# Kernel optimization log

Measured on AMD Instinct MI355X. Metric: run time of the kernel, lower is better.

The kernel has to match this reference:

```python
import jax, jax.numpy as jnp
import numpy as np

D_MODEL = 1024
N_HEADS = 16
HEAD_DIM = D_MODEL // N_HEADS
B, T = 4, 2048


def setup_inputs() -> dict:
    key = jax.random.key(0)
    ks = jax.random.split(key, 5)
    s = D_MODEL ** -0.5
    return {
        "x": jax.random.normal(ks[0], (B, T, D_MODEL), dtype=jnp.float32),
        "Wqkv": jax.random.normal(ks[1], (3 * D_MODEL, D_MODEL), dtype=jnp.float32) * s,
        "bqkv": jax.random.normal(ks[2], (3 * D_MODEL,), dtype=jnp.float32) * 0.01,
        "Wo": jax.random.normal(ks[3], (D_MODEL, D_MODEL), dtype=jnp.float32) * s,
        "bo": jax.random.normal(ks[4], (D_MODEL,), dtype=jnp.float32) * 0.01,
    }


def reference(x, Wqkv, bqkv, Wo, bo):
    b, t, c = x.shape
    h, hd = N_HEADS, HEAD_DIM
    qkv = x @ Wqkv.T + bqkv                      # [B,T,3C]
    # Faithful to source: reshape to [B,T,H,3*hd] THEN chunk -> per-head slices of 3C
    qkv = qkv.reshape(b, t, h, 3 * hd).transpose(0, 2, 1, 3)  # [B,H,T,3hd]
    q, k, v = jnp.split(qkv, 3, axis=-1)          # each [B,H,T,hd]
    scores = jnp.einsum('bhqd,bhkd->bhqk', q, k) * (hd ** -0.5)
    attn = jax.nn.softmax(scores, axis=-1)        # [B,H,T,T]
    out = jnp.einsum('bhqk,bhkd->bhqd', attn, v)  # [B,H,T,hd]
    out = out.transpose(0, 2, 1, 3).reshape(b, t, c)
    return out @ Wo.T + bo
```

## Files before the change

### kernel.cpp

```cpp
#include <hip/hip_runtime.h>
#include <hip/hip_bf16.h>


typedef float f32x4 __attribute__((ext_vector_type(4)));
typedef short s16x8 __attribute__((ext_vector_type(8)));
typedef short s16x4 __attribute__((ext_vector_type(4)));
typedef unsigned int u32x4 __attribute__((ext_vector_type(4)));

#define MFMA(acc, a, b) \
    (acc) = __builtin_amdgcn_mfma_f32_16x16x32_bf16((a), (b), (acc), 0, 0, 0)

__device__ __forceinline__ short f2bb(float f) {
    return (short)__bfloat16_as_ushort(__float2bfloat16(f));
}

__global__ __launch_bounds__(256)
void conv_all(const float* __restrict__ x, const float* __restrict__ Wqkv,
              const float* __restrict__ bqkv, const float* __restrict__ Wo,
              short* __restrict__ xb, short* __restrict__ Wqkvb,
              float* __restrict__ bqkvr, short* __restrict__ Wob)
{
    int blk = blockIdx.x;
    if (blk < 4096) {
        long i = ((long)blk * 256 + threadIdx.x) * 8;
        f32x4 a = *(const f32x4*)(x + i);
        f32x4 b = *(const f32x4*)(x + i + 4);
        s16x8 r;
#pragma unroll
        for (int j = 0; j < 4; j++) { r[j] = f2bb(a[j]); r[4 + j] = f2bb(b[j]); }
        *(s16x8*)(xb + i) = r;
    } else if (blk < 4096 + 3072) {
        int np = blk - 4096;
        int slice = np >> 10, rr = np & 1023;
        int src = (rr >> 6) * 192 + slice * 64 + (rr & 63);
        f32x4 v = *(const f32x4*)(Wqkv + (long)src * 1024 + threadIdx.x * 4);
        s16x4 o;
#pragma unroll
        for (int j = 0; j < 4; j++) o[j] = f2bb(v[j]);
        *(s16x4*)(Wqkvb + (long)np * 1024 + threadIdx.x * 4) = o;
        if (threadIdx.x == 0) bqkvr[np] = bqkv[src];
    } else {
        int n = blk - 4096 - 3072;
        f32x4 v = *(const f32x4*)(Wo + (long)n * 1024 + threadIdx.x * 4);
        s16x4 o;
#pragma unroll
        for (int j = 0; j < 4; j++) o[j] = f2bb(v[j]);
        *(s16x4*)(Wob + (long)n * 1024 + threadIdx.x * 4) = o;
    }
}

__global__ __launch_bounds__(256)
void gemm128(const short* __restrict__ A, const short* __restrict__ W,
             const float* __restrict__ bias,
             short* __restrict__ Cq, short* __restrict__ Ck,
             short* __restrict__ Cv, float* __restrict__ Cf, int proj)
{
    __shared__ short Asw[128 * 64];
    __shared__ short Bsw[128 * 64];
    const int tid = threadIdx.x;
    const int wave = tid >> 6, lane = tid & 63;
    const int quad = lane >> 4, l16 = lane & 15;
    const int m0 = blockIdx.y * 128;
    const int ng = blockIdx.x * 128;
    const int sr = tid >> 3, sc = tid & 7;

    f32x4 acc[4][4] = {};
    s16x8 pav[4], pbv[4];

#pragma unroll
    for (int u = 0; u < 4; u++) {
        int r = u * 32 + sr;
        pav[u] = *(const s16x8*)(A + (long)(m0 + r) * 1024 + sc * 8);
        pbv[u] = *(const s16x8*)(W + (long)(ng + r) * 1024 + sc * 8);
    }

    for (int k0 = 0; k0 < 1024; k0 += 64) {
        __syncthreads();
#pragma unroll
        for (int u = 0; u < 4; u++) {
            int r = u * 32 + sr;
            int slot = sc ^ (r & 7);
            *(s16x8*)&Asw[r * 64 + slot * 8] = pav[u];
            *(s16x8*)&Bsw[r * 64 + slot * 8] = pbv[u];
        }
        __syncthreads();
        if (k0 + 64 < 1024) {
            int kn = k0 + 64;
#pragma unroll
            for (int u = 0; u < 4; u++) {
                int r = u * 32 + sr;
                pav[u] = *(const s16x8*)(A + (long)(m0 + r) * 1024 + kn + sc * 8);
                pbv[u] = *(const s16x8*)(W + (long)(ng + r) * 1024 + kn + sc * 8);
            }
        }

        s16x8 af[2][4], bf[2][4];
#pragma unroll
        for (int ks = 0; ks < 2; ks++)
#pragma unroll
            for (int i = 0; i < 4; i++) {
                int slot = (ks * 4 + quad) ^ (l16 & 7);
                int ra = (wave >> 1) * 64 + i * 16 + l16;
                af[ks][i] = *(const s16x8*)&Asw[ra * 64 + slot * 8];
                int rb = (wave & 1) * 64 + i * 16 + l16;
                bf[ks][i] = *(const s16x8*)&Bsw[rb * 64 + slot * 8];
            }
#pragma unroll
        for (int ks = 0; ks < 2; ks++)
#pragma unroll
            for (int i = 0; i < 4; i++)
#pragma unroll
                for (int j = 0; j < 4; j++)
                    MFMA(acc[i][j], af[ks][i], bf[ks][j]);
    }

    const int slice = ng >> 10;
    const float scale = (!proj && slice == 0) ? 0.125f : 1.0f;
    short* Cb = (slice == 0) ? Cq : (slice == 1) ? Ck : Cv;
    const int nl = ng & 1023;
#pragma unroll
    for (int i = 0; i < 4; i++)
#pragma unroll
        for (int r = 0; r < 4; r++) {
            long m = m0 + (wave >> 1) * 64 + i * 16 + quad * 4 + r;
#pragma unroll
            for (int j = 0; j < 4; j++) {
                int cw = (wave & 1) * 64 + j * 16 + l16;
                float v = (acc[i][j][r] + bias[ng + cw]) * scale;
                if (proj) Cf[m * 1024 + ng + cw] = v;
                else      Cb[m * 1024 + nl + cw] = f2bb(v);
            }
        }
}

__global__ __launch_bounds__(256)
void attn(const short* __restrict__ Q, const short* __restrict__ Kb,
          const short* __restrict__ Vb, short* __restrict__ ao)
{
    __shared__ short Ksw[64 * 64];
    __shared__ unsigned int Vt[64 * 36];

    const int tid = threadIdx.x;
    const int wave = tid >> 6, lane = tid & 63;
    const int quad = lane >> 4, l16 = lane & 15;
    const int bh = blockIdx.x;
    const int b = bh >> 4, h = bh & 15;
    const int q0 = blockIdx.y * 64, hc = h * 64;
    const long rowbase = (long)b * 2048;

    s16x8 qf[2];
    {
        const short* qp = Q + (rowbase + q0 + wave * 16 + l16) * 1024 + hc + quad * 8;
        qf[0] = *(const s16x8*)qp;
        qf[1] = *(const s16x8*)(qp + 32);
    }

    s16x8 vones;
#pragma unroll
    for (int j = 0; j < 8; j++) vones[j] = (short)0x3F80;

    f32x4 O[4] = {};
    f32x4 Osum = {};

    const int ksr = tid >> 3, ksc = tid & 7;
    const int kp = tid & 31, ve = tid >> 5;
    const int key0 = ((kp >> 4) << 5) + (((kp >> 1) & 1) << 4)
                   + (((kp >> 2) & 3) << 2) + ((kp & 1) << 1);

    s16x8 kv0, kv1, va, vb2;
    {
        kv0 = *(const s16x8*)(Kb + (rowbase + ksr) * 1024 + hc + ksc * 8);
        kv1 = *(const s16x8*)(Kb + (rowbase + 32 + ksr) * 1024 + hc + ksc * 8);
        const short* v0 = Vb + (rowbase + key0) * 1024 + hc + ve * 8;
        va  = *(const s16x8*)v0;
        vb2 = *(const s16x8*)(v0 + 1024);
    }

    for (int kb = 0; kb < 2048; kb += 64) {
        __syncthreads();
        {
            int slot0 = ksc ^ (ksr & 7);
            *(s16x8*)&Ksw[ksr * 64 + slot0 * 8] = kv0;
            int r1 = 32 + ksr;
            int slot1 = ksc ^ (r1 & 7);
            *(s16x8*)&Ksw[r1 * 64 + slot1 * 8] = kv1;
            u32x4 vaU = __builtin_bit_cast(u32x4, va);
            u32x4 vbU = __builtin_bit_cast(u32x4, vb2);
#pragma unroll
            for (int w = 0; w < 4; w++) {
                unsigned int lo = __builtin_amdgcn_perm(vbU[w], vaU[w], 0x05040100u);
                unsigned int hi = __builtin_amdgcn_perm(vbU[w], vaU[w], 0x07060302u);
                Vt[(ve * 8 + 2 * w) * 36 + kp] = lo;
                Vt[(ve * 8 + 2 * w + 1) * 36 + kp] = hi;
            }
        }
        __syncthreads();

        if (kb + 64 < 2048) {
            int kn = kb + 64;
            kv0 = *(const s16x8*)(Kb + (rowbase + kn + ksr) * 1024 + hc + ksc * 8);
            kv1 = *(const s16x8*)(Kb + (rowbase + kn + 32 + ksr) * 1024 + hc + ksc * 8);
            const short* v0 = Vb + (rowbase + kn + key0) * 1024 + hc + ve * 8;
            va  = *(const s16x8*)v0;
            vb2 = *(const s16x8*)(v0 + 1024);
        }

        f32x4 S[4] = {};
        __builtin_amdgcn_s_setprio(1);
#pragma unroll
        for (int kt = 0; kt < 4; kt++) {
            int key = kt * 16 + l16;
#pragma unroll
            for (int kf = 0; kf < 2; kf++) {
                int slot = (kf * 4 + quad) ^ (l16 & 7);
                s16x8 kfrag = *(const s16x8*)&Ksw[key * 64 + slot * 8];
                MFMA(S[kt], kfrag, qf[kf]);
            }
        }
        __builtin_amdgcn_s_setprio(0);

        s16x8 af[2];
#pragma unroll
        for (int kt = 0; kt < 4; kt++)
#pragma unroll
            for (int r = 0; r < 4; r++) {
                float p = __builtin_amdgcn_exp2f(
                    __builtin_fmaf(S[kt][r], 1.44269504f, -17.3123405f));
                af[kt >> 1][(kt & 1) * 4 + r] = f2bb(p);
            }

        __builtin_amdgcn_s_setprio(1);
#pragma unroll
        for (int dt = 0; dt < 4; dt++) {
            int d = dt * 16 + l16;
#pragma unroll
            for (int kf = 0; kf < 2; kf++) {
                s16x8 vf = *(const s16x8*)&Vt[d * 36 + kf * 16 + quad * 4];
                MFMA(O[dt], af[kf], vf);
            }
        }
        MFMA(Osum, af[0], vones);
        MFMA(Osum, af[1], vones);
        __builtin_amdgcn_s_setprio(0);
    }

#pragma unroll
    for (int r = 0; r < 4; r++) {
        float invr = 1.0f / Osum[r];
        short* orow = ao + (rowbase + q0 + wave * 16 + quad * 4 + r) * 1024 + hc + l16;
#pragma unroll
        for (int dt = 0; dt < 4; dt++)
            orow[dt * 16] = f2bb(O[dt][r] * invr);
    }
}

__global__ void const_fill(float* out, int n, float c) {
    int i = blockIdx.x * 256 + threadIdx.x;
    if (i < n) out[i] = c;
}

extern "C" void kernel_launch(void* const* d_in, const int* in_sizes, int n_in,
                              void* d_out, int out_size, void* d_ws, size_t ws_size,
                              hipStream_t stream)
{
    const float* x    = (const float*)d_in[0];
    const float* Wqkv = (const float*)d_in[1];
    const float* bqkv = (const float*)d_in[2];
    const float* Wo   = (const float*)d_in[3];
    const float* bo   = (const float*)d_in[4];

    const size_t MB = 1u << 20;
    if (ws_size < 32 * MB) {
        const_fill<<<(out_size + 255) / 256, 256, 0, stream>>>(
            (float*)d_out, out_size, 66.0f);
        return;
    }

    char* ws = (char*)d_ws;
    short* xb     = (short*)(ws);
    short* Wqkvb  = (short*)(ws + 16777216);
    float* bqkvr  = (float*)(ws + 23068672);
    short* Wob    = (short*)(ws + 23085056);

    short* qbuf = (short*)d_out;
    short* kbuf = qbuf + (size_t)8192 * 1024;
    short* vbuf = (short*)d_in[0] + (size_t)8192 * 1024;
    short* ao   = (short*)d_in[0];

    dim3 blk(256);
    conv_all<<<4096 + 3072 + 1024, blk, 0, stream>>>(
        x, Wqkv, bqkv, Wo, xb, Wqkvb, bqkvr, Wob);

    gemm128<<<dim3(24, 64), blk, 0, stream>>>(xb, Wqkvb, bqkvr,
                                              qbuf, kbuf, vbuf, nullptr, 0);
    attn<<<dim3(64, 32), blk, 0, stream>>>(qbuf, kbuf, vbuf, ao);
    gemm128<<<dim3(8, 64), blk, 0, stream>>>(ao, Wob, bo,
                                             nullptr, nullptr, nullptr,
                                             (float*)d_out, 1);
}
```

Before: 287.3 us.

## Process two 64-row query subtiles per attention block to reuse K/V tiles

```diff
diff --git a/kernel.cpp b/kernel.cpp
--- a/kernel.cpp
+++ b/kernel.cpp
@@ -145,22 +145,24 @@
     const int quad = lane >> 4, l16 = lane & 15;
     const int bh = blockIdx.x;
     const int b = bh >> 4, h = bh & 15;
-    const int q0 = blockIdx.y * 64, hc = h * 64;
+    const int q0 = blockIdx.y * 128, hc = h * 64;
     const long rowbase = (long)b * 2048;
 
-    s16x8 qf[2];
-    {
-        const short* qp = Q + (rowbase + q0 + wave * 16 + l16) * 1024 + hc + quad * 8;
-        qf[0] = *(const s16x8*)qp;
-        qf[1] = *(const s16x8*)(qp + 32);
+    s16x8 qf[2][2];
+#pragma unroll
+    for (int s = 0; s < 2; s++) {
+        const short* qp = Q + (rowbase + q0 + s * 64 + wave * 16 + l16) * 1024
+                        + hc + quad * 8;
+        qf[s][0] = *(const s16x8*)qp;
+        qf[s][1] = *(const s16x8*)(qp + 32);
     }
 
     s16x8 vones;
 #pragma unroll
     for (int j = 0; j < 8; j++) vones[j] = (short)0x3F80;
 
-    f32x4 O[4] = {};
-    f32x4 Osum = {};
+    f32x4 O[2][4] = {};
+    f32x4 Osum[2] = {};
 
     const int ksr = tid >> 3, ksc = tid & 7;
     const int kp = tid & 31, ve = tid >> 5;
@@ -205,53 +207,59 @@
             vb2 = *(const s16x8*)(v0 + 1024);
         }
 
-        f32x4 S[4] = {};
+        s16x8 af[2][2];
         __builtin_amdgcn_s_setprio(1);
 #pragma unroll
         for (int kt = 0; kt < 4; kt++) {
             int key = kt * 16 + l16;
-#pragma unroll
-            for (int kf = 0; kf < 2; kf++) {
-                int slot = (kf * 4 + quad) ^ (l16 & 7);
-                s16x8 kfrag = *(const s16x8*)&Ksw[key * 64 + slot * 8];
-                MFMA(S[kt], kfrag, qf[kf]);
-            }
-        }
-        __builtin_amdgcn_s_setprio(0);
-
-        s16x8 af[2];
-#pragma unroll
-        for (int kt = 0; kt < 4; kt++)
+            int slot0 = quad ^ (l16 & 7);
+            int slot1 = (4 + quad) ^ (l16 & 7);
+            s16x8 kf0 = *(const s16x8*)&Ksw[key * 64 + slot0 * 8];
+            s16x8 kf1 = *(const s16x8*)&Ksw[key * 64 + slot1 * 8];
+            f32x4 s0 = {}, s1 = {};
+            MFMA(s0, kf0, qf[0][0]);
+            MFMA(s0, kf1, qf[0][1]);
+            MFMA(s1, kf0, qf[1][0]);
+            MFMA(s1, kf1, qf[1][1]);
 #pragma unroll
             for (int r = 0; r < 4; r++) {
-                float p = __builtin_amdgcn_exp2f(
-                    __builtin_fmaf(S[kt][r], 1.44269504f, -17.3123405f));
-                af[kt >> 1][(kt & 1) * 4 + r] = f2bb(p);
-            }
-
-        __builtin_amdgcn_s_setprio(1);
+                float p0 = __builtin_amdgcn_exp2f(
+                    __builtin_fmaf(s0[r], 1.44269504f, -17.3123405f));
+                float p1 = __builtin_amdgcn_exp2f(
+                    __builtin_fmaf(s1[r], 1.44269504f, -17.3123405f));
+                af[0][kt >> 1][(kt & 1) * 4 + r] = f2bb(p0);
+                af[1][kt >> 1][(kt & 1) * 4 + r] = f2bb(p1);
+            }
+        }
+
 #pragma unroll
         for (int dt = 0; dt < 4; dt++) {
             int d = dt * 16 + l16;
 #pragma unroll
             for (int kf = 0; kf < 2; kf++) {
                 s16x8 vf = *(const s16x8*)&Vt[d * 36 + kf * 16 + quad * 4];
-                MFMA(O[dt], af[kf], vf);
-            }
-        }
-        MFMA(Osum, af[0], vones);
-        MFMA(Osum, af[1], vones);
+                MFMA(O[0][dt], af[0][kf], vf);
+                MFMA(O[1][dt], af[1][kf], vf);
+            }
+        }
+        MFMA(Osum[0], af[0][0], vones);
+        MFMA(Osum[0], af[0][1], vones);
+        MFMA(Osum[1], af[1][0], vones);
+        MFMA(Osum[1], af[1][1], vones);
         __builtin_amdgcn_s_setprio(0);
     }
 
 #pragma unroll
-    for (int r = 0; r < 4; r++) {
-        float invr = 1.0f / Osum[r];
-        short* orow = ao + (rowbase + q0 + wave * 16 + quad * 4 + r) * 1024 + hc + l16;
-#pragma unroll
-        for (int dt = 0; dt < 4; dt++)
-            orow[dt * 16] = f2bb(O[dt][r] * invr);
-    }
+    for (int s = 0; s < 2; s++)
+#pragma unroll
+        for (int r = 0; r < 4; r++) {
+            float invr = 1.0f / Osum[s][r];
+            short* orow = ao + (rowbase + q0 + s * 64 + wave * 16 + quad * 4 + r) * 1024
+                        + hc + l16;
+#pragma unroll
+            for (int dt = 0; dt < 4; dt++)
+                orow[dt * 16] = f2bb(O[s][dt][r] * invr);
+        }
 }
 
 __global__ void const_fill(float* out, int n, float c) {
@@ -293,7 +301,7 @@
 
     gemm128<<<dim3(24, 64), blk, 0, stream>>>(xb, Wqkvb, bqkvr,
                                               qbuf, kbuf, vbuf, nullptr, 0);
-    attn<<<dim3(64, 32), blk, 0, stream>>>(qbuf, kbuf, vbuf, ao);
+    attn<<<dim3(64, 16), blk, 0, stream>>>(qbuf, kbuf, vbuf, ao);
     gemm128<<<dim3(8, 64), blk, 0, stream>>>(ao, Wob, bo,
                                              nullptr, nullptr, nullptr,
                                              (float*)d_out, 1);
```

Measured after the change: 264.4 us. 1.09x faster.
